# Performance work log

Hardware: AMD Instinct MI355X
Metric: run time of the kernel (lower is better)

## Reference

```python
import jax, jax.numpy as jnp
import numpy as np

N_NODES = 50000


def setup_inputs() -> dict:
    key = jax.random.key(0)
    ks = jax.random.split(key, 10)
    E = 800000
    x = jax.random.normal(ks[0], (N_NODES, 256), dtype=jnp.float32)
    src = jax.random.randint(ks[1], (E,), 0, N_NODES, dtype=jnp.int32)
    dst = jax.random.randint(ks[2], (E,), 0, N_NODES, dtype=jnp.int32)
    w = jax.random.uniform(ks[3], (E,), dtype=jnp.float32)
    W1 = jax.random.normal(ks[4], (256, 128), dtype=jnp.float32) / np.sqrt(256)
    b1 = jnp.zeros((128,), dtype=jnp.float32)
    W2 = jax.random.normal(ks[5], (128, 128), dtype=jnp.float32) / np.sqrt(128)
    b2 = jnp.zeros((128,), dtype=jnp.float32)
    W3 = jax.random.normal(ks[6], (128, 64), dtype=jnp.float32) / np.sqrt(128)
    b3 = jnp.zeros((64,), dtype=jnp.float32)
    return {"x": x, "src": src, "dst": dst, "w": w,
            "W1": W1, "b1": b1, "W2": W2, "b2": b2, "W3": W3, "b3": b3}


def _graph_conv(x, src, dst, w, W, b):
    # dense projection then edge-weighted gather-multiply-scatter-sum
    h = x @ W + b                              # [N, d_out]
    msgs = h[src] * w[:, None]                 # [E, d_out] per-edge messages
    return jax.ops.segment_sum(msgs, dst, num_segments=N_NODES)


def reference(x, src, dst, w, W1, b1, W2, b2, W3, b3):
    h = _graph_conv(x, src, dst, w, W1, b1)
    h = jax.nn.relu(h)
    h = _graph_conv(h, src, dst, w, W2, b2)
    h = jax.nn.relu(h)
    h = _graph_conv(h, src, dst, w, W3, b3)
    return h
```

## Files before the change

kernel.cpp:

```cpp
#include <hip/hip_runtime.h>
#include <hip/hip_bf16.h>

#define N_NODES 50000
#define BSHIFT  6
#define BSIZE   64
#define NBUCK   ((N_NODES + BSIZE - 1) / BSIZE)
#define BIN_BLOCKS 256

using short8  = __attribute__((ext_vector_type(8))) short;
using short4v = __attribute__((ext_vector_type(4))) short;
using floatx4 = __attribute__((ext_vector_type(4))) float;

__device__ inline short f32_to_bf16_bits(float f) {
    __hip_bfloat16 h = __float2bfloat16(f);
    return *reinterpret_cast<short*>(&h);
}

template<int K, int N, bool A_F32>
__global__ __launch_bounds__(256) void mfma_gemm(const void* __restrict__ Araw,
                                                 const short* __restrict__ WTf,
                                                 const float* __restrict__ bias,
                                                 short* __restrict__ C, int M)
{
    constexpr int KS = K / 32;
    constexpr int CT = N / 32;
    constexpr int LK = K + 8;

    __shared__ __align__(16) short As[64][LK];

    const int tid  = threadIdx.x;
    const int wave = tid >> 6;
    const int lane = tid & 63;
    const int l15  = lane & 15;
    const int lk   = (lane >> 4) * 8;
    const int wr   = wave >> 1;
    const int wc   = wave & 1;
    const int r0   = blockIdx.x * 64;

    if (A_F32) {
        const float* Af = (const float*)Araw;
#pragma unroll
        for (int it = 0; it < 64 * (K / 4) / 256; ++it) {
            const int idx = it * 256 + tid;
            const int row = idx / (K / 4);
            const int c4  = idx % (K / 4);
            const int gr  = min(r0 + row, M - 1);
            const float4 v = *reinterpret_cast<const float4*>(&Af[(size_t)gr * K + c4 * 4]);
            short4v s;
            s[0] = f32_to_bf16_bits(v.x); s[1] = f32_to_bf16_bits(v.y);
            s[2] = f32_to_bf16_bits(v.z); s[3] = f32_to_bf16_bits(v.w);
            *reinterpret_cast<short4v*>(&As[row][c4 * 4]) = s;
        }
    } else {
        const short* Ab = (const short*)Araw;
#pragma unroll
        for (int it = 0; it < 64 * (K / 8) / 256; ++it) {
            const int idx = it * 256 + tid;
            const int row = idx / (K / 8);
            const int c8  = idx % (K / 8);
            const int gr  = min(r0 + row, M - 1);
            const short8 v = *reinterpret_cast<const short8*>(&Ab[(size_t)gr * K + c8 * 8]);
            *reinterpret_cast<short8*>(&As[row][c8 * 8]) = v;
        }
    }
    __syncthreads();

    float bv[CT];
#pragma unroll
    for (int t = 0; t < CT; ++t) bv[t] = bias[wc * (N / 2) + t * 16 + l15];

    floatx4 acc[2][CT];
#pragma unroll
    for (int rt = 0; rt < 2; ++rt)
#pragma unroll
        for (int t = 0; t < CT; ++t) acc[rt][t] = (floatx4){0.f, 0.f, 0.f, 0.f};

#pragma unroll
    for (int ks = 0; ks < KS; ++ks) {
        short8 b[CT];
#pragma unroll
        for (int t = 0; t < CT; ++t) {
            const int tg = wc * CT + t;
            b[t] = *reinterpret_cast<const short8*>(&WTf[((size_t)(tg * KS + ks) * 64 + lane) * 8]);
        }
        short8 a[2];
#pragma unroll
        for (int rt = 0; rt < 2; ++rt)
            a[rt] = *reinterpret_cast<const short8*>(&As[wr * 32 + rt * 16 + l15][ks * 32 + lk]);
#pragma unroll
        for (int rt = 0; rt < 2; ++rt)
#pragma unroll
            for (int t = 0; t < CT; ++t)
                acc[rt][t] = __builtin_amdgcn_mfma_f32_16x16x32_bf16(a[rt], b[t], acc[rt][t], 0, 0, 0);
    }

    const int rowg = (lane >> 4) * 4;
#pragma unroll
    for (int rt = 0; rt < 2; ++rt)
#pragma unroll
        for (int t = 0; t < CT; ++t)
#pragma unroll
            for (int j = 0; j < 4; ++j) {
                const int gr = r0 + wr * 32 + rt * 16 + rowg + j;
                if (gr < M)
                    C[(size_t)gr * N + wc * (N / 2) + t * 16 + l15] =
                        f32_to_bf16_bits(acc[rt][t][j] + bv[t]);
            }
}

__device__ inline void wt_frag(const float* __restrict__ W, short* __restrict__ out,
                               int K, int N, int u)
{
    const int lane = u & 63;
    const int rest = u >> 6;
    const int KS   = K >> 5;
    const int ks   = rest % KS;
    const int tg   = rest / KS;
    const int n    = tg * 16 + (lane & 15);
    const int kb   = ks * 32 + (lane >> 4) * 8;
    short8 s;
#pragma unroll
    for (int e = 0; e < 8; ++e) s[e] = f32_to_bf16_bits(W[(size_t)(kb + e) * N + n]);
    *reinterpret_cast<short8*>(&out[(size_t)u * 8]) = s;
}

__global__ __launch_bounds__(256) void wt_all(const float* __restrict__ W1, short* __restrict__ WT1,
                                              const float* __restrict__ W2, short* __restrict__ WT2,
                                              const float* __restrict__ W3, short* __restrict__ WT3)
{
    const int u = blockIdx.x * 256 + threadIdx.x;
    if (u < 4096)             wt_frag(W1, WT1, 256, 128, u);
    else if (u < 4096 + 2048) wt_frag(W2, WT2, 128, 128, u - 4096);
    else if (u < 7168)        wt_frag(W3, WT3, 128, 64,  u - 6144);
}


__global__ __launch_bounds__(256) void bin_hist(const int* __restrict__ dst,
                                                int* __restrict__ hist_g, int E)
{
    __shared__ int hist[NBUCK];
    for (int t = threadIdx.x; t < NBUCK; t += 256) hist[t] = 0;
    __syncthreads();
    const int chunk = (E + BIN_BLOCKS - 1) / BIN_BLOCKS;
    const int beg = blockIdx.x * chunk;
    const int end = min(beg + chunk, E);
    for (int i = beg + threadIdx.x; i < end; i += 256)
        atomicAdd(&hist[dst[i] >> BSHIFT], 1);
    __syncthreads();
    for (int t = threadIdx.x; t < NBUCK; t += 256)
        hist_g[blockIdx.x * NBUCK + t] = hist[t];
}

__global__ __launch_bounds__(256) void bin_scan_blocks(const int* __restrict__ hist_g,
                                                       int* __restrict__ blockbase,
                                                       int* __restrict__ tot)
{
    __shared__ int s[BIN_BLOCKS];
    const int b = blockIdx.x;
    const int t = threadIdx.x;
    const int v = hist_g[t * NBUCK + b];
    s[t] = v;
    __syncthreads();
#pragma unroll
    for (int off = 1; off < BIN_BLOCKS; off <<= 1) {
        const int tmp = (t >= off) ? s[t - off] : 0;
        __syncthreads();
        s[t] += tmp;
        __syncthreads();
    }
    blockbase[t * NBUCK + b] = s[t] - v;
    if (t == BIN_BLOCKS - 1) tot[b] = s[t];
}

__global__ __launch_bounds__(256) void bin_scan_tot(const int* __restrict__ tot,
                                                    int* __restrict__ bucket_base)
{
    __shared__ int psum[256];
    const int t = threadIdx.x;
    int vals[4];
    int s = 0;
#pragma unroll
    for (int j = 0; j < 4; ++j) {
        const int idx = t * 4 + j;
        vals[j] = (idx < NBUCK) ? tot[idx] : 0;
        s += vals[j];
    }
    psum[t] = s;
    __syncthreads();
#pragma unroll
    for (int off = 1; off < 256; off <<= 1) {
        const int tmp = (t >= off) ? psum[t - off] : 0;
        __syncthreads();
        psum[t] += tmp;
        __syncthreads();
    }
    int run = psum[t] - s;
#pragma unroll
    for (int j = 0; j < 4; ++j) {
        const int idx = t * 4 + j;
        if (idx < NBUCK) bucket_base[idx] = run;
        run += vals[j];
    }
    if (t == 255) bucket_base[NBUCK] = run;
}

__global__ __launch_bounds__(256) void bin_write(const int* __restrict__ src,
                                                 const int* __restrict__ dst,
                                                 const float* __restrict__ w,
                                                 const int* __restrict__ blockbase,
                                                 const int* __restrict__ bucket_base,
                                                 int2* __restrict__ tmp, int E)
{
    __shared__ int cur[NBUCK];
    for (int t = threadIdx.x; t < NBUCK; t += 256)
        cur[t] = bucket_base[t] + blockbase[blockIdx.x * NBUCK + t];
    __syncthreads();
    const int chunk = (E + BIN_BLOCKS - 1) / BIN_BLOCKS;
    const int beg = blockIdx.x * chunk;
    const int end = min(beg + chunk, E);
    for (int i = beg + threadIdx.x; i < end; i += 256) {
        const int d = dst[i];
        const int pos = atomicAdd(&cur[d >> BSHIFT], 1);
        tmp[pos] = make_int2((src[i] << BSHIFT) | (d & (BSIZE - 1)), __float_as_int(w[i]));
    }
}

__global__ __launch_bounds__(256) void fine_fill2(const int2* __restrict__ tmp,
                                                  const int* __restrict__ bucket_base,
                                                  int2* __restrict__ csr_ew,
                                                  int* __restrict__ row_ptr)
{
    __shared__ int hist[BSIZE];
    __shared__ int basel[BSIZE];
    const int b    = blockIdx.x;
    const int t    = threadIdx.x;
    const int rbeg = bucket_base[b];
    const int rend = bucket_base[b + 1];

    if (t < BSIZE) hist[t] = 0;
    __syncthreads();
    for (int i = rbeg + t; i < rend; i += 256)
        atomicAdd(&hist[((unsigned)tmp[i].x) & (BSIZE - 1)], 1);
    __syncthreads();

    if (t < BSIZE) {
        const int v = hist[t];
        int inc = v;
#pragma unroll
        for (int off = 1; off < BSIZE; off <<= 1) {
            const int u = __shfl_up(inc, off, 64);
            if (t >= off) inc += u;
        }
        const int excl = rbeg + inc - v;
        basel[t] = excl;
        const int node = (b << BSHIFT) + t;
        if (node < N_NODES) row_ptr[node] = excl;
        if (b == NBUCK - 1 && t == 0) row_ptr[N_NODES] = bucket_base[NBUCK];
    }
    __syncthreads();

    for (int i = rbeg + t; i < rend; i += 256) {
        const int2 e = tmp[i];
        const unsigned ex = (unsigned)e.x;
        const int pos = atomicAdd(&basel[ex & (BSIZE - 1)], 1);
        csr_ew[pos] = make_int2((int)(ex >> BSHIFT), e.y);
    }
}

template<bool RELU>
__global__ __launch_bounds__(256) void pull128_bf(const unsigned int* __restrict__ h,
                                                  const int* __restrict__ row_ptr,
                                                  const int2* __restrict__ csr_ew,
                                                  unsigned int* __restrict__ out, int n_nodes)
{
    const int wave = threadIdx.x >> 6;
    const int lane = threadIdx.x & 63;
    const int node = blockIdx.x * 4 + wave;
    if (node >= n_nodes) return;

    const int beg = row_ptr[node];
    const int end = row_ptr[node + 1];

    float ax0 = 0.f, ay0 = 0.f, ax1 = 0.f, ay1 = 0.f;
    float ax2 = 0.f, ay2 = 0.f, ax3 = 0.f, ay3 = 0.f;

    for (int c = beg; c < end; c += 64) {
        const int idx = c + lane;
        int2 ew = make_int2(0, 0);
        if (idx < end) ew = csr_ew[idx];
        const int cnt = min(64, end - c);

        int j = 0;
        for (; j + 4 <= cnt; j += 4) {
            const int   s0 = __shfl(ew.x, j);
            const int   s1 = __shfl(ew.x, j + 1);
            const int   s2 = __shfl(ew.x, j + 2);
            const int   s3 = __shfl(ew.x, j + 3);
            const float w0 = __int_as_float(__shfl(ew.y, j));
            const float w1 = __int_as_float(__shfl(ew.y, j + 1));
            const float w2 = __int_as_float(__shfl(ew.y, j + 2));
            const float w3 = __int_as_float(__shfl(ew.y, j + 3));
            const unsigned int p0 = h[(size_t)s0 * 64 + lane];
            const unsigned int p1 = h[(size_t)s1 * 64 + lane];
            const unsigned int p2 = h[(size_t)s2 * 64 + lane];
            const unsigned int p3 = h[(size_t)s3 * 64 + lane];
            ax0 = fmaf(__int_as_float(p0 << 16), w0, ax0);
            ay0 = fmaf(__int_as_float(p0 & 0xffff0000u), w0, ay0);
            ax1 = fmaf(__int_as_float(p1 << 16), w1, ax1);
            ay1 = fmaf(__int_as_float(p1 & 0xffff0000u), w1, ay1);
            ax2 = fmaf(__int_as_float(p2 << 16), w2, ax2);
            ay2 = fmaf(__int_as_float(p2 & 0xffff0000u), w2, ay2);
            ax3 = fmaf(__int_as_float(p3 << 16), w3, ax3);
            ay3 = fmaf(__int_as_float(p3 & 0xffff0000u), w3, ay3);
        }
        for (; j < cnt; ++j) {
            const int   s0 = __shfl(ew.x, j);
            const float w0 = __int_as_float(__shfl(ew.y, j));
            const unsigned int p0 = h[(size_t)s0 * 64 + lane];
            ax0 = fmaf(__int_as_float(p0 << 16), w0, ax0);
            ay0 = fmaf(__int_as_float(p0 & 0xffff0000u), w0, ay0);
        }
    }

    float ax = (ax0 + ax1) + (ax2 + ax3);
    float ay = (ay0 + ay1) + (ay2 + ay3);
    if (RELU) { ax = fmaxf(ax, 0.f); ay = fmaxf(ay, 0.f); }
    const unsigned int lo = (unsigned short)f32_to_bf16_bits(ax);
    const unsigned int hi = (unsigned short)f32_to_bf16_bits(ay);
    out[(size_t)node * 64 + lane] = lo | (hi << 16);
}

__global__ __launch_bounds__(256) void pull64_bf(const unsigned int* __restrict__ h,
                                                 const int* __restrict__ row_ptr,
                                                 const int2* __restrict__ csr_ew,
                                                 float2* __restrict__ out, int n_nodes)
{
    const int wave = threadIdx.x >> 6;
    const int lane = threadIdx.x & 63;
    const int half = lane >> 5;
    const int l32  = lane & 31;
    const int node = blockIdx.x * 8 + wave * 2 + half;
    if (node >= n_nodes) return;

    const int beg = row_ptr[node];
    const int end = row_ptr[node + 1];

    float ax0 = 0.f, ay0 = 0.f, ax1 = 0.f, ay1 = 0.f;
    float ax2 = 0.f, ay2 = 0.f, ax3 = 0.f, ay3 = 0.f;

    for (int c = beg; c < end; c += 32) {
        const int idx = c + l32;
        int2 ew = make_int2(0, 0);
        if (idx < end) ew = csr_ew[idx];
        const int cnt = min(32, end - c);

        int j = 0;
        for (; j + 4 <= cnt; j += 4) {
            const int   s0 = __shfl(ew.x, j, 32);
            const int   s1 = __shfl(ew.x, j + 1, 32);
            const int   s2 = __shfl(ew.x, j + 2, 32);
            const int   s3 = __shfl(ew.x, j + 3, 32);
            const float w0 = __int_as_float(__shfl(ew.y, j, 32));
            const float w1 = __int_as_float(__shfl(ew.y, j + 1, 32));
            const float w2 = __int_as_float(__shfl(ew.y, j + 2, 32));
            const float w3 = __int_as_float(__shfl(ew.y, j + 3, 32));
            const unsigned int p0 = h[(size_t)s0 * 32 + l32];
            const unsigned int p1 = h[(size_t)s1 * 32 + l32];
            const unsigned int p2 = h[(size_t)s2 * 32 + l32];
            const unsigned int p3 = h[(size_t)s3 * 32 + l32];
            ax0 = fmaf(__int_as_float(p0 << 16), w0, ax0);
            ay0 = fmaf(__int_as_float(p0 & 0xffff0000u), w0, ay0);
            ax1 = fmaf(__int_as_float(p1 << 16), w1, ax1);
            ay1 = fmaf(__int_as_float(p1 & 0xffff0000u), w1, ay1);
            ax2 = fmaf(__int_as_float(p2 << 16), w2, ax2);
            ay2 = fmaf(__int_as_float(p2 & 0xffff0000u), w2, ay2);
            ax3 = fmaf(__int_as_float(p3 << 16), w3, ax3);
            ay3 = fmaf(__int_as_float(p3 & 0xffff0000u), w3, ay3);
        }
        for (; j < cnt; ++j) {
            const int   s0 = __shfl(ew.x, j, 32);
            const float w0 = __int_as_float(__shfl(ew.y, j, 32));
            const unsigned int p0 = h[(size_t)s0 * 32 + l32];
            ax0 = fmaf(__int_as_float(p0 << 16), w0, ax0);
            ay0 = fmaf(__int_as_float(p0 & 0xffff0000u), w0, ay0);
        }
    }

    const float ax = (ax0 + ax1) + (ax2 + ax3);
    const float ay = (ay0 + ay1) + (ay2 + ay3);
    out[(size_t)node * 32 + l32] = make_float2(ax, ay);
}

extern "C" void kernel_launch(void* const* d_in, const int* in_sizes, int n_in,
                              void* d_out, int out_size, void* d_ws, size_t ws_size,
                              hipStream_t stream)
{
    const float* x   = (const float*)d_in[0];
    const int*   src = (const int*)  d_in[1];
    const int*   dst = (const int*)  d_in[2];
    const float* w   = (const float*)d_in[3];
    const float* W1  = (const float*)d_in[4];
    const float* b1  = (const float*)d_in[5];
    const float* W2  = (const float*)d_in[6];
    const float* b2  = (const float*)d_in[7];
    const float* W3  = (const float*)d_in[8];
    const float* b3  = (const float*)d_in[9];

    const int E = in_sizes[1];
    const int M = N_NODES;

    short* hA  = (short*)d_ws;
    short* hB  = hA + (size_t)M * 128;
    short* WT1 = hB + (size_t)M * 128;
    short* WT2 = WT1 + 128 * 256;
    short* WT3 = WT2 + 128 * 128;
    int2*  csr_ew      = (int2*)(WT3 + 64 * 128);
    int2*  tmp_ew      = csr_ew + E;
    int*   row_ptr     = (int*)(tmp_ew + E);
    int*   hist_g      = row_ptr + 50048;
    int*   blockbase   = hist_g + 200704;
    int*   bucket_base = blockbase + 200704;
    int*   tot         = bucket_base + 1024;

    const int gemm_blocks = (M + 63) / 64;

    wt_all<<<28, 256, 0, stream>>>(W1, WT1, W2, WT2, W3, WT3);
    bin_hist<<<BIN_BLOCKS, 256, 0, stream>>>(dst, hist_g, E);
    bin_scan_blocks<<<NBUCK, BIN_BLOCKS, 0, stream>>>(hist_g, blockbase, tot);
    bin_scan_tot<<<1, 256, 0, stream>>>(tot, bucket_base);
    bin_write<<<BIN_BLOCKS, 256, 0, stream>>>(src, dst, w, blockbase, bucket_base, tmp_ew, E);
    fine_fill2<<<NBUCK, 256, 0, stream>>>(tmp_ew, bucket_base, csr_ew, row_ptr);

    mfma_gemm<256, 128, true><<<gemm_blocks, 256, 0, stream>>>(x, WT1, b1, hA, M);
    pull128_bf<true><<<(M + 3) / 4, 256, 0, stream>>>((const unsigned int*)hA, row_ptr, csr_ew,
                                                      (unsigned int*)hB, M);
    mfma_gemm<128, 128, false><<<gemm_blocks, 256, 0, stream>>>(hB, WT2, b2, hA, M);
    pull128_bf<true><<<(M + 3) / 4, 256, 0, stream>>>((const unsigned int*)hA, row_ptr, csr_ew,
                                                      (unsigned int*)hB, M);
    mfma_gemm<128, 64, false><<<gemm_blocks, 256, 0, stream>>>(hB, WT3, b3, hA, M);
    pull64_bf<<<(M + 7) / 8, 256, 0, stream>>>((const unsigned int*)hA, row_ptr, csr_ew,
                                               (float2*)d_out, M);
}
```

Before: 161.2 us.

## Pack CSR edges as 16-bit src plus bf16 weight and unroll gather by 8

The CSR edge array now packs the source index (high 16 bits) and a bf16-rounded edge weight (low 16 bits) into a single 32-bit word, halving edge-list traffic and shuffles in the pull kernels. The pull loops gather 8 neighbours per iteration with 8 independent accumulators to expose more memory-level parallelism, using predicated zero entries in place of a scalar tail loop. The packing relies on node indices below 65536 (N_NODES=50000 fits) and reduces weight precision to bf16. Padding entries point at node 0 with weight zero, which adds harmless extra loads for short rows.

```diff
diff --git a/kernel.cpp b/kernel.cpp
--- a/kernel.cpp
+++ b/kernel.cpp
@@ -227,7 +227,7 @@
 
 __global__ __launch_bounds__(256) void fine_fill2(const int2* __restrict__ tmp,
                                                   const int* __restrict__ bucket_base,
-                                                  int2* __restrict__ csr_ew,
+                                                  unsigned int* __restrict__ csr_ew,
                                                   int* __restrict__ row_ptr)
 {
     __shared__ int hist[BSIZE];
@@ -263,14 +263,15 @@
         const int2 e = tmp[i];
         const unsigned ex = (unsigned)e.x;
         const int pos = atomicAdd(&basel[ex & (BSIZE - 1)], 1);
-        csr_ew[pos] = make_int2((int)(ex >> BSHIFT), e.y);
+        const unsigned wb = (unsigned short)f32_to_bf16_bits(__int_as_float(e.y));
+        csr_ew[pos] = ((ex >> BSHIFT) << 16) | wb;
     }
 }
 
 template<bool RELU>
 __global__ __launch_bounds__(256) void pull128_bf(const unsigned int* __restrict__ h,
                                                   const int* __restrict__ row_ptr,
-                                                  const int2* __restrict__ csr_ew,
+                                                  const unsigned int* __restrict__ csr_ew,
                                                   unsigned int* __restrict__ out, int n_nodes)
 {
     const int wave = threadIdx.x >> 6;
@@ -281,58 +282,46 @@
     const int beg = row_ptr[node];
     const int end = row_ptr[node + 1];
 
-    float ax0 = 0.f, ay0 = 0.f, ax1 = 0.f, ay1 = 0.f;
-    float ax2 = 0.f, ay2 = 0.f, ax3 = 0.f, ay3 = 0.f;
+    float ax[8], ay[8];
+#pragma unroll
+    for (int u = 0; u < 8; ++u) { ax[u] = 0.f; ay[u] = 0.f; }
 
     for (int c = beg; c < end; c += 64) {
         const int idx = c + lane;
-        int2 ew = make_int2(0, 0);
-        if (idx < end) ew = csr_ew[idx];
+        const unsigned ew = (idx < end) ? csr_ew[idx] : 0u;
         const int cnt = min(64, end - c);
 
-        int j = 0;
-        for (; j + 4 <= cnt; j += 4) {
-            const int   s0 = __shfl(ew.x, j);
-            const int   s1 = __shfl(ew.x, j + 1);
-            const int   s2 = __shfl(ew.x, j + 2);
-            const int   s3 = __shfl(ew.x, j + 3);
-            const float w0 = __int_as_float(__shfl(ew.y, j));
-            const float w1 = __int_as_float(__shfl(ew.y, j + 1));
-            const float w2 = __int_as_float(__shfl(ew.y, j + 2));
-            const float w3 = __int_as_float(__shfl(ew.y, j + 3));
-            const unsigned int p0 = h[(size_t)s0 * 64 + lane];
-            const unsigned int p1 = h[(size_t)s1 * 64 + lane];
-            const unsigned int p2 = h[(size_t)s2 * 64 + lane];
-            const unsigned int p3 = h[(size_t)s3 * 64 + lane];
-            ax0 = fmaf(__int_as_float(p0 << 16), w0, ax0);
-            ay0 = fmaf(__int_as_float(p0 & 0xffff0000u), w0, ay0);
-            ax1 = fmaf(__int_as_float(p1 << 16), w1, ax1);
-            ay1 = fmaf(__int_as_float(p1 & 0xffff0000u), w1, ay1);
-            ax2 = fmaf(__int_as_float(p2 << 16), w2, ax2);
-            ay2 = fmaf(__int_as_float(p2 & 0xffff0000u), w2, ay2);
-            ax3 = fmaf(__int_as_float(p3 << 16), w3, ax3);
-            ay3 = fmaf(__int_as_float(p3 & 0xffff0000u), w3, ay3);
-        }
-        for (; j < cnt; ++j) {
-            const int   s0 = __shfl(ew.x, j);
-            const float w0 = __int_as_float(__shfl(ew.y, j));
-            const unsigned int p0 = h[(size_t)s0 * 64 + lane];
-            ax0 = fmaf(__int_as_float(p0 << 16), w0, ax0);
-            ay0 = fmaf(__int_as_float(p0 & 0xffff0000u), w0, ay0);
-        }
-    }
-
-    float ax = (ax0 + ax1) + (ax2 + ax3);
-    float ay = (ay0 + ay1) + (ay2 + ay3);
-    if (RELU) { ax = fmaxf(ax, 0.f); ay = fmaxf(ay, 0.f); }
-    const unsigned int lo = (unsigned short)f32_to_bf16_bits(ax);
-    const unsigned int hi = (unsigned short)f32_to_bf16_bits(ay);
+        for (int j = 0; j < cnt; j += 8) {
+            unsigned e[8];
+#pragma unroll
+            for (int u = 0; u < 8; ++u) {
+                const unsigned v = __shfl(ew, j + u);
+                e[u] = (j + u < cnt) ? v : 0u;
+            }
+            unsigned p[8];
+#pragma unroll
+            for (int u = 0; u < 8; ++u)
+                p[u] = h[(size_t)(e[u] >> 16) * 64 + lane];
+#pragma unroll
+            for (int u = 0; u < 8; ++u) {
+                const float wv = __int_as_float(e[u] << 16);
+                ax[u] = fmaf(__int_as_float(p[u] << 16), wv, ax[u]);
+                ay[u] = fmaf(__int_as_float(p[u] & 0xffff0000u), wv, ay[u]);
+            }
+        }
+    }
+
+    float axs = ((ax[0] + ax[1]) + (ax[2] + ax[3])) + ((ax[4] + ax[5]) + (ax[6] + ax[7]));
+    float ays = ((ay[0] + ay[1]) + (ay[2] + ay[3])) + ((ay[4] + ay[5]) + (ay[6] + ay[7]));
+    if (RELU) { axs = fmaxf(axs, 0.f); ays = fmaxf(ays, 0.f); }
+    const unsigned lo = (unsigned short)f32_to_bf16_bits(axs);
+    const unsigned hi = (unsigned short)f32_to_bf16_bits(ays);
     out[(size_t)node * 64 + lane] = lo | (hi << 16);
 }
 
 __global__ __launch_bounds__(256) void pull64_bf(const unsigned int* __restrict__ h,
                                                  const int* __restrict__ row_ptr,
-                                                 const int2* __restrict__ csr_ew,
+                                                 const unsigned int* __restrict__ csr_ew,
                                                  float2* __restrict__ out, int n_nodes)
 {
     const int wave = threadIdx.x >> 6;
@@ -345,50 +334,38 @@
     const int beg = row_ptr[node];
     const int end = row_ptr[node + 1];
 
-    float ax0 = 0.f, ay0 = 0.f, ax1 = 0.f, ay1 = 0.f;
-    float ax2 = 0.f, ay2 = 0.f, ax3 = 0.f, ay3 = 0.f;
+    float ax[8], ay[8];
+#pragma unroll
+    for (int u = 0; u < 8; ++u) { ax[u] = 0.f; ay[u] = 0.f; }
 
     for (int c = beg; c < end; c += 32) {
         const int idx = c + l32;
-        int2 ew = make_int2(0, 0);
-        if (idx < end) ew = csr_ew[idx];
+        const unsigned ew = (idx < end) ? csr_ew[idx] : 0u;
         const int cnt = min(32, end - c);
 
-        int j = 0;
-        for (; j + 4 <= cnt; j += 4) {
-            const int   s0 = __shfl(ew.x, j, 32);
-            const int   s1 = __shfl(ew.x, j + 1, 32);
-            const int   s2 = __shfl(ew.x, j + 2, 32);
-            const int   s3 = __shfl(ew.x, j + 3, 32);
-            const float w0 = __int_as_float(__shfl(ew.y, j, 32));
-            const float w1 = __int_as_float(__shfl(ew.y, j + 1, 32));
-            const float w2 = __int_as_float(__shfl(ew.y, j + 2, 32));
-            const float w3 = __int_as_float(__shfl(ew.y, j + 3, 32));
-            const unsigned int p0 = h[(size_t)s0 * 32 + l32];
-            const unsigned int p1 = h[(size_t)s1 * 32 + l32];
-            const unsigned int p2 = h[(size_t)s2 * 32 + l32];
-            const unsigned int p3 = h[(size_t)s3 * 32 + l32];
-            ax0 = fmaf(__int_as_float(p0 << 16), w0, ax0);
-            ay0 = fmaf(__int_as_float(p0 & 0xffff0000u), w0, ay0);
-            ax1 = fmaf(__int_as_float(p1 << 16), w1, ax1);
-            ay1 = fmaf(__int_as_float(p1 & 0xffff0000u), w1, ay1);
-            ax2 = fmaf(__int_as_float(p2 << 16), w2, ax2);
-            ay2 = fmaf(__int_as_float(p2 & 0xffff0000u), w2, ay2);
-            ax3 = fmaf(__int_as_float(p3 << 16), w3, ax3);
-            ay3 = fmaf(__int_as_float(p3 & 0xffff0000u), w3, ay3);
-        }
-        for (; j < cnt; ++j) {
-            const int   s0 = __shfl(ew.x, j, 32);
-            const float w0 = __int_as_float(__shfl(ew.y, j, 32));
-            const unsigned int p0 = h[(size_t)s0 * 32 + l32];
-            ax0 = fmaf(__int_as_float(p0 << 16), w0, ax0);
-            ay0 = fmaf(__int_as_float(p0 & 0xffff0000u), w0, ay0);
-        }
-    }
-
-    const float ax = (ax0 + ax1) + (ax2 + ax3);
-    const float ay = (ay0 + ay1) + (ay2 + ay3);
-    out[(size_t)node * 32 + l32] = make_float2(ax, ay);
+        for (int j = 0; j < cnt; j += 8) {
+            unsigned e[8];
+#pragma unroll
+            for (int u = 0; u < 8; ++u) {
+                const unsigned v = __shfl(ew, j + u, 32);
+                e[u] = (j + u < cnt) ? v : 0u;
+            }
+            unsigned p[8];
+#pragma unroll
+            for (int u = 0; u < 8; ++u)
+                p[u] = h[(size_t)(e[u] >> 16) * 32 + l32];
+#pragma unroll
+            for (int u = 0; u < 8; ++u) {
+                const float wv = __int_as_float(e[u] << 16);
+                ax[u] = fmaf(__int_as_float(p[u] << 16), wv, ax[u]);
+                ay[u] = fmaf(__int_as_float(p[u] & 0xffff0000u), wv, ay[u]);
+            }
+        }
+    }
+
+    const float axs = ((ax[0] + ax[1]) + (ax[2] + ax[3])) + ((ax[4] + ax[5]) + (ax[6] + ax[7]));
+    const float ays = ((ay[0] + ay[1]) + (ay[2] + ay[3])) + ((ay[4] + ay[5]) + (ay[6] + ay[7]));
+    out[(size_t)node * 32 + l32] = make_float2(axs, ays);
 }
 
 extern "C" void kernel_launch(void* const* d_in, const int* in_sizes, int n_in,
@@ -414,8 +391,8 @@
     short* WT1 = hB + (size_t)M * 128;
     short* WT2 = WT1 + 128 * 256;
     short* WT3 = WT2 + 128 * 128;
-    int2*  csr_ew      = (int2*)(WT3 + 64 * 128);
-    int2*  tmp_ew      = csr_ew + E;
+    unsigned int* csr_ew = (unsigned int*)(WT3 + 64 * 128);
+    int2*  tmp_ew      = (int2*)(csr_ew + ((E + 1) & ~1));
     int*   row_ptr     = (int*)(tmp_ew + E);
     int*   hist_g      = row_ptr + 50048;
     int*   blockbase   = hist_g + 200704;
```

New measurement: 153.3 us. -4.9%, faster.
